# Kernel tuning notes

Hardware: AMD Instinct MI355X
Metric: run time of the kernel (lower is better)

The kernel has to match this reference:

```python
import jax, jax.numpy as jnp
import numpy as np

H = 8       # n_heads
N = 128     # n_vars
HEAD = 64   # per-head dim (== __init__ dim)


def setup_inputs() -> dict:
    key = jax.random.key(0)
    k0, k1, k2, k3, k4 = jax.random.split(key, 5)
    B, L = 4, 8192
    D = H * HEAD
    x = jax.random.normal(k0, (B, L, D), dtype=jnp.float32)
    # nn.Linear default init: U(-1/sqrt(fan_in), 1/sqrt(fan_in)), fan_in = HEAD
    s = 1.0 / np.sqrt(HEAD)
    w1 = jax.random.uniform(k1, (HEAD, HEAD), jnp.float32, -s, s)
    b1 = jax.random.uniform(k2, (HEAD,), jnp.float32, -s, s)
    w2 = jax.random.uniform(k3, (HEAD, HEAD), jnp.float32, -s, s)
    b2 = jax.random.uniform(k4, (HEAD,), jnp.float32, -s, s)
    return {"x": x, "w1": w1, "b1": b1, "w2": w2, "b2": b2}


def reference(x, w1, b1, w2, b2):
    B, L, D = x.shape
    P = L // N  # patches per variable
    # (B,L,D) -> (B,H,L,HEAD) -> (B,H,N,P,HEAD)
    xh = x.reshape(B, L, H, HEAD).transpose(0, 2, 1, 3).reshape(B, H, N, P, HEAD)
    q = xh @ w1.T + b1  # proj_1
    k = xh @ w2.T + b2  # proj_2
    # per (b,h,patch) NxN adjacency over variables
    adj = jax.nn.gelu(jnp.einsum('bhixd,bhjxd->bhxij', q, k), approximate=False)
    adj = jax.nn.softmax(adj, axis=-1)
    # dropout is identity in eval mode; F.normalize(p=1): divide by max(L1, eps)
    adj = adj / jnp.maximum(jnp.sum(jnp.abs(adj), axis=-1, keepdims=True), 1e-12)
    out = jnp.einsum('bhxij,bhjxd->bixhd', adj, xh)  # (B,N,P,H,HEAD)
    return out.reshape(B, L, H * HEAD)
```

## Files before the change

### kernel.cpp

```cpp
#include <hip/hip_runtime.h>
#include <math.h>


namespace {
constexpr int H = 8, NV = 128, HEAD = 64, B = 4, L = 8192;
constexpr int P = L / NV;
constexpr int D = H * HEAD;
constexpr int RS = P * D;

constexpr int XT_S = 136;
constexpr int XH_S = 72;
constexpr int TA_S = 72;

typedef _Float16 half8  __attribute__((ext_vector_type(8)));
typedef _Float16 half4h __attribute__((ext_vector_type(4)));
typedef _Float16 half2v __attribute__((ext_vector_type(2)));
typedef __fp16   fp16x2 __attribute__((ext_vector_type(2)));
typedef float    floatx4 __attribute__((ext_vector_type(4)));

__device__ __forceinline__ floatx4 mfma16(half8 a, half8 b, floatx4 c) {
    return __builtin_amdgcn_mfma_f32_16x16x32_f16(a, b, c, 0, 0, 0);
}

__device__ __forceinline__ half8 cvt8(float4 a, float4 b) {
    fp16x2 p0 = __builtin_amdgcn_cvt_pkrtz(a.x, a.y);
    fp16x2 p1 = __builtin_amdgcn_cvt_pkrtz(a.z, a.w);
    fp16x2 p2 = __builtin_amdgcn_cvt_pkrtz(b.x, b.y);
    fp16x2 p3 = __builtin_amdgcn_cvt_pkrtz(b.z, b.w);
    half8 r;
    r[0] = (_Float16)p0[0]; r[1] = (_Float16)p0[1];
    r[2] = (_Float16)p1[0]; r[3] = (_Float16)p1[1];
    r[4] = (_Float16)p2[0]; r[5] = (_Float16)p2[1];
    r[6] = (_Float16)p3[0]; r[7] = (_Float16)p3[1];
    return r;
}

__device__ __forceinline__ float& vslot(_Float16* xt, int j) {
    return ((float*)(xt + (size_t)(j >> 2) * XT_S + 128))[j & 3];
}

__global__ __launch_bounds__(256) void pack_g(
    const float* __restrict__ w1, const float* __restrict__ w2,
    const float* __restrict__ b1, const float* __restrict__ b2,
    _Float16* __restrict__ gth, float* __restrict__ g1f,
    float* __restrict__ g2f, float* __restrict__ cf)
{
    const int t = threadIdx.x;
    if (blockIdx.x == 16) {
        if (t < 64) {
            float a = 0.f;
            #pragma unroll 8
            for (int n = 0; n < 64; ++n) a = fmaf(w1[n * 64 + t], b2[n], a);
            g1f[t] = a;
        } else if (t < 128) {
            const int d = t - 64;
            float a = 0.f;
            #pragma unroll 8
            for (int n = 0; n < 64; ++n) a = fmaf(w2[n * 64 + d], b1[n], a);
            g2f[d] = a;
        } else if (t == 128) {
            float a = 0.f;
            for (int n = 0; n < 64; ++n) a = fmaf(b1[n], b2[n], a);
            cf[0] = a;
        }
        return;
    }
    const int gid = blockIdx.x * 256 + t;
    const int d = gid & 63, e = gid >> 6;
    float a = 0.f;
    #pragma unroll 8
    for (int n = 0; n < 64; ++n) a = fmaf(w1[n * 64 + d], w2[n * 64 + e], a);
    gth[e * 64 + d] = (_Float16)a;
}

__global__ __launch_bounds__(256, 3) void space_graph_mfma5(
    const float* __restrict__ x, const _Float16* __restrict__ gth,
    const float* __restrict__ g1f, const float* __restrict__ g2f,
    const float* __restrict__ cf, float* __restrict__ out)
{
    __shared__ _Float16 lds[64 * XT_S + NV * XH_S + NV * TA_S];
    _Float16* Xt = lds;
    _Float16* Xh = lds + 64 * XT_S;
    _Float16* TA = Xh + NV * XH_S;

    const int t    = threadIdx.x;
    const int lane = t & 63;
    const int w    = t >> 6;
    const int col  = lane & 15;
    const int quad = lane >> 4;

    const int blk = blockIdx.x;
    const int p = blk & (P - 1);
    const int h = (blk >> 6) & (H - 1);
    const int b = blk >> 9;
    const size_t base = ((size_t)b * L + (size_t)p) * D + (size_t)h * HEAD;

    {
        const int c  = t & 15;
        const int tt = t >> 4;
        #pragma unroll
        for (int it = 0; it < 4; ++it) {
            const int j0 = 2 * (tt + 16 * it);
            const float4 v0 = *(const float4*)(x + base + (size_t)j0 * RS + c * 4);
            const float4 v1 = *(const float4*)(x + base + (size_t)(j0 + 1) * RS + c * 4);
            const float va[4] = {v0.x, v0.y, v0.z, v0.w};
            const float vb[4] = {v1.x, v1.y, v1.z, v1.w};
            half4h ra, rb;
            #pragma unroll
            for (int q = 0; q < 4; ++q) {
                const _Float16 ha = (_Float16)va[q];
                const _Float16 hb = (_Float16)vb[q];
                ra[q] = ha; rb[q] = hb;
                half2v pr; pr[0] = ha; pr[1] = hb;
                *(half2v*)&Xt[(4 * c + q) * XT_S + j0] = pr;
            }
            *(half4h*)&Xh[(size_t)j0 * XH_S + 4 * c] = ra;
            *(half4h*)&Xh[(size_t)(j0 + 1) * XH_S + 4 * c] = rb;
        }
    }

    floatx4 tacc[2][4];
    #pragma unroll
    for (int mt = 0; mt < 2; ++mt)
        #pragma unroll
        for (int nt = 0; nt < 4; ++nt) tacc[mt][nt] = (floatx4)0.0f;

    half8 axf[2][2];
    float up[2] = {0.f, 0.f}, vp[2] = {0.f, 0.f};
    #pragma unroll
    for (int ks = 0; ks < 2; ++ks) {
        const float4 ga = *(const float4*)(g1f + quad * 8 + 32 * ks);
        const float4 gb = *(const float4*)(g1f + quad * 8 + 32 * ks + 4);
        const float4 ha = *(const float4*)(g2f + quad * 8 + 32 * ks);
        const float4 hb = *(const float4*)(g2f + quad * 8 + 32 * ks + 4);
        #pragma unroll
        for (int mt = 0; mt < 2; ++mt) {
            const int row = 32 * w + 16 * mt + col;
            const float* src = x + base + (size_t)row * RS + quad * 8 + 32 * ks;
            const float4 v0 = *(const float4*)src;
            const float4 v1 = *(const float4*)(src + 4);
            axf[mt][ks] = cvt8(v0, v1);
            up[mt] += v0.x * ga.x + v0.y * ga.y + v0.z * ga.z + v0.w * ga.w
                    + v1.x * gb.x + v1.y * gb.y + v1.z * gb.z + v1.w * gb.w;
            vp[mt] += v0.x * ha.x + v0.y * ha.y + v0.z * ha.z + v0.w * ha.w
                    + v1.x * hb.x + v1.y * hb.y + v1.z * hb.z + v1.w * hb.w;
        }
    }

    #pragma unroll
    for (int ks = 0; ks < 2; ++ks)
        #pragma unroll
        for (int nt = 0; nt < 4; ++nt) {
            const half8 gb8 = *(const half8*)&gth[(col + 16 * nt) * HEAD + quad * 8 + 32 * ks];
            #pragma unroll
            for (int mt = 0; mt < 2; ++mt)
                tacc[mt][nt] = mfma16(axf[mt][ks], gb8, tacc[mt][nt]);
        }

    float ureg[2];
    #pragma unroll
    for (int mt = 0; mt < 2; ++mt) {
        float uu = up[mt]; uu += __shfl_xor(uu, 16); uu += __shfl_xor(uu, 32);
        float vv = vp[mt]; vv += __shfl_xor(vv, 16); vv += __shfl_xor(vv, 32);
        ureg[mt] = uu;
        if (quad == 0) vslot(Xt, 32 * w + 16 * mt + col) = vv;
    }

    #pragma unroll
    for (int mt = 0; mt < 2; ++mt)
        #pragma unroll
        for (int r = 0; r < 4; ++r) {
            const int R = 32 * w + 16 * mt + quad * 4 + r;
            _Float16* trow = &TA[R * TA_S + col];
            #pragma unroll
            for (int nt = 0; nt < 4; ++nt)
                trow[nt * 16] = (_Float16)(tacc[mt][nt][r]);
        }
    __syncthreads();

    const float cc = cf[0];
    float ucr[2][4];
    #pragma unroll
    for (int mt = 0; mt < 2; ++mt)
        #pragma unroll
        for (int r = 0; r < 4; ++r)
            ucr[mt][r] = __shfl(ureg[mt], quad * 4 + r) + cc;
    float vrow[8];
    #pragma unroll
    for (int nt = 0; nt < 8; ++nt) vrow[nt] = vslot(Xt, col + 16 * nt);

    floatx4 sacc[2][8];
    #pragma unroll
    for (int mt = 0; mt < 2; ++mt)
        #pragma unroll
        for (int nt = 0; nt < 8; ++nt)
            #pragma unroll
            for (int r = 0; r < 4; ++r)
                sacc[mt][nt][r] = ucr[mt][r] + vrow[nt];

    #pragma unroll
    for (int ks = 0; ks < 2; ++ks) {
        half8 taf[2];
        #pragma unroll
        for (int mt = 0; mt < 2; ++mt)
            taf[mt] = *(const half8*)&TA[(32 * w + 16 * mt + col) * TA_S + quad * 8 + 32 * ks];
        #pragma unroll
        for (int nt = 0; nt < 8; ++nt) {
            const half8 xb = *(const half8*)&Xh[(col + 16 * nt) * XH_S + quad * 8 + 32 * ks];
            #pragma unroll
            for (int mt = 0; mt < 2; ++mt)
                sacc[mt][nt] = mfma16(taf[mt], xb, sacc[mt][nt]);
        }
    }

    #pragma unroll
    for (int mt = 0; mt < 2; ++mt)
        #pragma unroll
        for (int r = 0; r < 4; ++r) {
            float wv[8]; float rs = 0.f;
            #pragma unroll
            for (int nt = 0; nt < 8; ++nt) {
                const float s  = sacc[mt][nt][r];
                const float u  = s * fmaf(s * s, 0.035677408137f, 0.7978845608f);
                const float em = __expf(-2.0f * u);
                const float g  = s * __builtin_amdgcn_rcpf(1.0f + em);
                const float e  = __expf(g);
                wv[nt] = e; rs += e;
            }
            rs += __shfl_xor(rs, 1); rs += __shfl_xor(rs, 2);
            rs += __shfl_xor(rs, 4); rs += __shfl_xor(rs, 8);
            const float inv = __builtin_amdgcn_rcpf(rs);
            #pragma unroll
            for (int nt = 0; nt < 8; ++nt) sacc[mt][nt][r] = wv[nt] * inv;
        }

    #pragma unroll
    for (int mt = 0; mt < 2; ++mt)
        #pragma unroll
        for (int r = 0; r < 4; ++r) {
            const int R = 32 * w + 16 * mt + quad * 4 + r;
            _Float16* arow = &TA[R * TA_S + col];
            #pragma unroll
            for (int nt = 0; nt < 4; ++nt)
                arow[nt * 16] = (_Float16)(sacc[mt][nt][r]);
        }

    floatx4 oacc[2][4];
    #pragma unroll
    for (int mt = 0; mt < 2; ++mt)
        #pragma unroll
        for (int nt = 0; nt < 4; ++nt) oacc[mt][nt] = (floatx4)0.0f;

    #pragma unroll
    for (int kh = 0; kh < 2; ++kh) {
        half8 aaf[2];
        #pragma unroll
        for (int mt = 0; mt < 2; ++mt)
            aaf[mt] = *(const half8*)&TA[(32 * w + 16 * mt + col) * TA_S + quad * 8 + 32 * kh];
        #pragma unroll
        for (int nt = 0; nt < 4; ++nt) {
            const half8 xb = *(const half8*)&Xt[(col + 16 * nt) * XT_S + quad * 8 + 32 * kh];
            #pragma unroll
            for (int mt = 0; mt < 2; ++mt)
                oacc[mt][nt] = mfma16(aaf[mt], xb, oacc[mt][nt]);
        }
    }

    #pragma unroll
    for (int mt = 0; mt < 2; ++mt)
        #pragma unroll
        for (int r = 0; r < 4; ++r) {
            const int R = 32 * w + 16 * mt + quad * 4 + r;
            _Float16* arow = &TA[R * TA_S + col];
            #pragma unroll
            for (int nt = 4; nt < 8; ++nt)
                arow[(nt - 4) * 16] = (_Float16)(sacc[mt][nt][r]);
        }

    #pragma unroll
    for (int kh = 0; kh < 2; ++kh) {
        half8 aaf[2];
        #pragma unroll
        for (int mt = 0; mt < 2; ++mt)
            aaf[mt] = *(const half8*)&TA[(32 * w + 16 * mt + col) * TA_S + quad * 8 + 32 * kh];
        #pragma unroll
        for (int nt = 0; nt < 4; ++nt) {
            const half8 xb = *(const half8*)&Xt[(col + 16 * nt) * XT_S + quad * 8 + 32 * (kh + 2)];
            #pragma unroll
            for (int mt = 0; mt < 2; ++mt)
                oacc[mt][nt] = mfma16(aaf[mt], xb, oacc[mt][nt]);
        }
    }

    #pragma unroll
    for (int mt = 0; mt < 2; ++mt)
        #pragma unroll
        for (int r = 0; r < 4; ++r) {
            const int i = 32 * w + 16 * mt + quad * 4 + r;
            float* orow = out + base + (size_t)i * RS + col;
            #pragma unroll
            for (int nt = 0; nt < 4; ++nt)
                orow[nt * 16] = oacc[mt][nt][r];
        }
}
}

extern "C" void kernel_launch(void* const* d_in, const int* in_sizes, int n_in,
                              void* d_out, int out_size, void* d_ws, size_t ws_size,
                              hipStream_t stream) {
    const float* x  = (const float*)d_in[0];
    const float* w1 = (const float*)d_in[1];
    const float* b1 = (const float*)d_in[2];
    const float* w2 = (const float*)d_in[3];
    const float* b2 = (const float*)d_in[4];
    float* out = (float*)d_out;

    _Float16* gth = (_Float16*)d_ws;
    float* g1f = (float*)((char*)d_ws + 8192);
    float* g2f = g1f + 64;
    float* cf  = g2f + 64;

    hipLaunchKernelGGL(pack_g, dim3(17), dim3(256), 0, stream,
                       w1, w2, b1, b2, gth, g1f, g2f, cf);
    hipLaunchKernelGGL(space_graph_mfma5, dim3(B * H * P), dim3(256), 0, stream,
                       x, gth, g1f, g2f, cf, out);
}
```

Baseline: 142.3 us.

## Use 512-thread blocks with one 16-row tile per wave and exp2-based GELU

Each block now runs 8 waves, and each wave handles a single 16-row M tile instead of two. This halves per-thread accumulator registers and aims to raise occupancy and latency hiding. The GELU-tanh plus softmax exponent is rewritten with exp2 and pre-folded log2e constants to save multiplies. The trade-off is less MFMA work per wave against more waves sharing the same LDS tile per block.

```diff
diff --git a/kernel.cpp b/kernel.cpp
--- a/kernel.cpp
+++ b/kernel.cpp
@@ -73,7 +73,7 @@
     gth[e * 64 + d] = (_Float16)a;
 }
 
-__global__ __launch_bounds__(256, 3) void space_graph_mfma5(
+__global__ __launch_bounds__(512, 6) void space_graph_mfma6(
     const float* __restrict__ x, const _Float16* __restrict__ gth,
     const float* __restrict__ g1f, const float* __restrict__ g2f,
     const float* __restrict__ cf, float* __restrict__ out)
@@ -99,8 +99,8 @@
         const int c  = t & 15;
         const int tt = t >> 4;
         #pragma unroll
-        for (int it = 0; it < 4; ++it) {
-            const int j0 = 2 * (tt + 16 * it);
+        for (int it = 0; it < 2; ++it) {
+            const int j0 = 2 * (tt + 32 * it);
             const float4 v0 = *(const float4*)(x + base + (size_t)j0 * RS + c * 4);
             const float4 v1 = *(const float4*)(x + base + (size_t)(j0 + 1) * RS + c * 4);
             const float va[4] = {v0.x, v0.y, v0.z, v0.w};
@@ -119,32 +119,27 @@
         }
     }
 
-    floatx4 tacc[2][4];
-    #pragma unroll
-    for (int mt = 0; mt < 2; ++mt)
-        #pragma unroll
-        for (int nt = 0; nt < 4; ++nt) tacc[mt][nt] = (floatx4)0.0f;
-
-    half8 axf[2][2];
-    float up[2] = {0.f, 0.f}, vp[2] = {0.f, 0.f};
+    floatx4 tacc[4];
+    #pragma unroll
+    for (int nt = 0; nt < 4; ++nt) tacc[nt] = (floatx4)0.0f;
+
+    half8 axf[2];
+    float up = 0.f, vp = 0.f;
+    const int arow0 = 16 * w + col;
     #pragma unroll
     for (int ks = 0; ks < 2; ++ks) {
         const float4 ga = *(const float4*)(g1f + quad * 8 + 32 * ks);
         const float4 gb = *(const float4*)(g1f + quad * 8 + 32 * ks + 4);
         const float4 ha = *(const float4*)(g2f + quad * 8 + 32 * ks);
         const float4 hb = *(const float4*)(g2f + quad * 8 + 32 * ks + 4);
-        #pragma unroll
-        for (int mt = 0; mt < 2; ++mt) {
-            const int row = 32 * w + 16 * mt + col;
-            const float* src = x + base + (size_t)row * RS + quad * 8 + 32 * ks;
-            const float4 v0 = *(const float4*)src;
-            const float4 v1 = *(const float4*)(src + 4);
-            axf[mt][ks] = cvt8(v0, v1);
-            up[mt] += v0.x * ga.x + v0.y * ga.y + v0.z * ga.z + v0.w * ga.w
-                    + v1.x * gb.x + v1.y * gb.y + v1.z * gb.z + v1.w * gb.w;
-            vp[mt] += v0.x * ha.x + v0.y * ha.y + v0.z * ha.z + v0.w * ha.w
-                    + v1.x * hb.x + v1.y * hb.y + v1.z * hb.z + v1.w * hb.w;
-        }
+        const float* src = x + base + (size_t)arow0 * RS + quad * 8 + 32 * ks;
+        const float4 v0 = *(const float4*)src;
+        const float4 v1 = *(const float4*)(src + 4);
+        axf[ks] = cvt8(v0, v1);
+        up += v0.x * ga.x + v0.y * ga.y + v0.z * ga.z + v0.w * ga.w
+            + v1.x * gb.x + v1.y * gb.y + v1.z * gb.z + v1.w * gb.w;
+        vp += v0.x * ha.x + v0.y * ha.y + v0.z * ha.z + v0.w * ha.w
+            + v1.x * hb.x + v1.y * hb.y + v1.z * hb.z + v1.w * hb.w;
     }
 
     #pragma unroll
@@ -152,156 +147,122 @@
         #pragma unroll
         for (int nt = 0; nt < 4; ++nt) {
             const half8 gb8 = *(const half8*)&gth[(col + 16 * nt) * HEAD + quad * 8 + 32 * ks];
-            #pragma unroll
-            for (int mt = 0; mt < 2; ++mt)
-                tacc[mt][nt] = mfma16(axf[mt][ks], gb8, tacc[mt][nt]);
-        }
-
-    float ureg[2];
-    #pragma unroll
-    for (int mt = 0; mt < 2; ++mt) {
-        float uu = up[mt]; uu += __shfl_xor(uu, 16); uu += __shfl_xor(uu, 32);
-        float vv = vp[mt]; vv += __shfl_xor(vv, 16); vv += __shfl_xor(vv, 32);
-        ureg[mt] = uu;
-        if (quad == 0) vslot(Xt, 32 * w + 16 * mt + col) = vv;
-    }
-
-    #pragma unroll
-    for (int mt = 0; mt < 2; ++mt)
-        #pragma unroll
-        for (int r = 0; r < 4; ++r) {
-            const int R = 32 * w + 16 * mt + quad * 4 + r;
-            _Float16* trow = &TA[R * TA_S + col];
-            #pragma unroll
-            for (int nt = 0; nt < 4; ++nt)
-                trow[nt * 16] = (_Float16)(tacc[mt][nt][r]);
-        }
+            tacc[nt] = mfma16(axf[ks], gb8, tacc[nt]);
+        }
+
+    float ureg;
+    {
+        float uu = up; uu += __shfl_xor(uu, 16); uu += __shfl_xor(uu, 32);
+        float vv = vp; vv += __shfl_xor(vv, 16); vv += __shfl_xor(vv, 32);
+        ureg = uu;
+        if (quad == 0) vslot(Xt, arow0) = vv;
+    }
+
+    #pragma unroll
+    for (int r = 0; r < 4; ++r) {
+        const int R = 16 * w + quad * 4 + r;
+        _Float16* trow = &TA[R * TA_S + col];
+        #pragma unroll
+        for (int nt = 0; nt < 4; ++nt)
+            trow[nt * 16] = (_Float16)(tacc[nt][r]);
+    }
     __syncthreads();
 
     const float cc = cf[0];
-    float ucr[2][4];
-    #pragma unroll
-    for (int mt = 0; mt < 2; ++mt)
+    float ucr[4];
+    #pragma unroll
+    for (int r = 0; r < 4; ++r)
+        ucr[r] = __shfl(ureg, quad * 4 + r) + cc;
+    float vrow[8];
+    #pragma unroll
+    for (int nt = 0; nt < 8; ++nt) vrow[nt] = vslot(Xt, col + 16 * nt);
+
+    floatx4 sacc[8];
+    #pragma unroll
+    for (int nt = 0; nt < 8; ++nt)
         #pragma unroll
         for (int r = 0; r < 4; ++r)
-            ucr[mt][r] = __shfl(ureg[mt], quad * 4 + r) + cc;
-    float vrow[8];
-    #pragma unroll
-    for (int nt = 0; nt < 8; ++nt) vrow[nt] = vslot(Xt, col + 16 * nt);
-
-    floatx4 sacc[2][8];
-    #pragma unroll
-    for (int mt = 0; mt < 2; ++mt)
-        #pragma unroll
-        for (int nt = 0; nt < 8; ++nt)
-            #pragma unroll
-            for (int r = 0; r < 4; ++r)
-                sacc[mt][nt][r] = ucr[mt][r] + vrow[nt];
+            sacc[nt][r] = ucr[r] + vrow[nt];
 
     #pragma unroll
     for (int ks = 0; ks < 2; ++ks) {
-        half8 taf[2];
-        #pragma unroll
-        for (int mt = 0; mt < 2; ++mt)
-            taf[mt] = *(const half8*)&TA[(32 * w + 16 * mt + col) * TA_S + quad * 8 + 32 * ks];
+        const half8 taf = *(const half8*)&TA[arow0 * TA_S + quad * 8 + 32 * ks];
         #pragma unroll
         for (int nt = 0; nt < 8; ++nt) {
             const half8 xb = *(const half8*)&Xh[(col + 16 * nt) * XH_S + quad * 8 + 32 * ks];
-            #pragma unroll
-            for (int mt = 0; mt < 2; ++mt)
-                sacc[mt][nt] = mfma16(taf[mt], xb, sacc[mt][nt]);
-        }
-    }
-
-    #pragma unroll
-    for (int mt = 0; mt < 2; ++mt)
-        #pragma unroll
-        for (int r = 0; r < 4; ++r) {
-            float wv[8]; float rs = 0.f;
-            #pragma unroll
-            for (int nt = 0; nt < 8; ++nt) {
-                const float s  = sacc[mt][nt][r];
-                const float u  = s * fmaf(s * s, 0.035677408137f, 0.7978845608f);
-                const float em = __expf(-2.0f * u);
-                const float g  = s * __builtin_amdgcn_rcpf(1.0f + em);
-                const float e  = __expf(g);
-                wv[nt] = e; rs += e;
-            }
-            rs += __shfl_xor(rs, 1); rs += __shfl_xor(rs, 2);
-            rs += __shfl_xor(rs, 4); rs += __shfl_xor(rs, 8);
-            const float inv = __builtin_amdgcn_rcpf(rs);
-            #pragma unroll
-            for (int nt = 0; nt < 8; ++nt) sacc[mt][nt][r] = wv[nt] * inv;
-        }
-
-    #pragma unroll
-    for (int mt = 0; mt < 2; ++mt)
-        #pragma unroll
-        for (int r = 0; r < 4; ++r) {
-            const int R = 32 * w + 16 * mt + quad * 4 + r;
-            _Float16* arow = &TA[R * TA_S + col];
-            #pragma unroll
-            for (int nt = 0; nt < 4; ++nt)
-                arow[nt * 16] = (_Float16)(sacc[mt][nt][r]);
-        }
-
-    floatx4 oacc[2][4];
-    #pragma unroll
-    for (int mt = 0; mt < 2; ++mt)
-        #pragma unroll
-        for (int nt = 0; nt < 4; ++nt) oacc[mt][nt] = (floatx4)0.0f;
+            sacc[nt] = mfma16(taf, xb, sacc[nt]);
+        }
+    }
+
+    #pragma unroll
+    for (int r = 0; r < 4; ++r) {
+        float wv[8]; float rs = 0.f;
+        #pragma unroll
+        for (int nt = 0; nt < 8; ++nt) {
+            const float s   = sacc[nt][r];
+            const float pl  = fmaf(s * s, -0.10294310f, -2.3022157f);
+            const float em  = __builtin_amdgcn_exp2f(s * pl);
+            const float rr  = __builtin_amdgcn_rcpf(1.0f + em);
+            const float e   = __builtin_amdgcn_exp2f((s * 1.44269504f) * rr);
+            wv[nt] = e; rs += e;
+        }
+        rs += __shfl_xor(rs, 1); rs += __shfl_xor(rs, 2);
+        rs += __shfl_xor(rs, 4); rs += __shfl_xor(rs, 8);
+        const float inv = __builtin_amdgcn_rcpf(rs);
+        #pragma unroll
+        for (int nt = 0; nt < 8; ++nt) sacc[nt][r] = wv[nt] * inv;
+    }
+
+    #pragma unroll
+    for (int r = 0; r < 4; ++r) {
+        const int R = 16 * w + quad * 4 + r;
+        _Float16* arow = &TA[R * TA_S + col];
+        #pragma unroll
+        for (int nt = 0; nt < 4; ++nt)
+            arow[nt * 16] = (_Float16)(sacc[nt][r]);
+    }
+
+    floatx4 oacc[4];
+    #pragma unroll
+    for (int nt = 0; nt < 4; ++nt) oacc[nt] = (floatx4)0.0f;
 
     #pragma unroll
     for (int kh = 0; kh < 2; ++kh) {
-        half8 aaf[2];
-        #pragma unroll
-        for (int mt = 0; mt < 2; ++mt)
-            aaf[mt] = *(const half8*)&TA[(32 * w + 16 * mt + col) * TA_S + quad * 8 + 32 * kh];
+        const half8 aaf = *(const half8*)&TA[arow0 * TA_S + quad * 8 + 32 * kh];
         #pragma unroll
         for (int nt = 0; nt < 4; ++nt) {
             const half8 xb = *(const half8*)&Xt[(col + 16 * nt) * XT_S + quad * 8 + 32 * kh];
-            #pragma unroll
-            for (int mt = 0; mt < 2; ++mt)
-                oacc[mt][nt] = mfma16(aaf[mt], xb, oacc[mt][nt]);
-        }
-    }
-
-    #pragma unroll
-    for (int mt = 0; mt < 2; ++mt)
-        #pragma unroll
-        for (int r = 0; r < 4; ++r) {
-            const int R = 32 * w + 16 * mt + quad * 4 + r;
-            _Float16* arow = &TA[R * TA_S + col];
-            #pragma unroll
-            for (int nt = 4; nt < 8; ++nt)
-                arow[(nt - 4) * 16] = (_Float16)(sacc[mt][nt][r]);
-        }
+            oacc[nt] = mfma16(aaf, xb, oacc[nt]);
+        }
+    }
+
+    #pragma unroll
+    for (int r = 0; r < 4; ++r) {
+        const int R = 16 * w + quad * 4 + r;
+        _Float16* arow = &TA[R * TA_S + col];
+        #pragma unroll
+        for (int nt = 4; nt < 8; ++nt)
+            arow[(nt - 4) * 16] = (_Float16)(sacc[nt][r]);
+    }
 
     #pragma unroll
     for (int kh = 0; kh < 2; ++kh) {
-        half8 aaf[2];
-        #pragma unroll
-        for (int mt = 0; mt < 2; ++mt)
-            aaf[mt] = *(const half8*)&TA[(32 * w + 16 * mt + col) * TA_S + quad * 8 + 32 * kh];
+        const half8 aaf = *(const half8*)&TA[arow0 * TA_S + quad * 8 + 32 * kh];
         #pragma unroll
         for (int nt = 0; nt < 4; ++nt) {
             const half8 xb = *(const half8*)&Xt[(col + 16 * nt) * XT_S + quad * 8 + 32 * (kh + 2)];
-            #pragma unroll
-            for (int mt = 0; mt < 2; ++mt)
-                oacc[mt][nt] = mfma16(aaf[mt], xb, oacc[mt][nt]);
-        }
-    }
-
-    #pragma unroll
-    for (int mt = 0; mt < 2; ++mt)
-        #pragma unroll
-        for (int r = 0; r < 4; ++r) {
-            const int i = 32 * w + 16 * mt + quad * 4 + r;
-            float* orow = out + base + (size_t)i * RS + col;
-            #pragma unroll
-            for (int nt = 0; nt < 4; ++nt)
-                orow[nt * 16] = oacc[mt][nt][r];
-        }
+            oacc[nt] = mfma16(aaf, xb, oacc[nt]);
+        }
+    }
+
+    #pragma unroll
+    for (int r = 0; r < 4; ++r) {
+        const int i = 16 * w + quad * 4 + r;
+        float* orow = out + base + (size_t)i * RS + col;
+        #pragma unroll
+        for (int nt = 0; nt < 4; ++nt)
+            orow[nt * 16] = oacc[nt][r];
+    }
 }
 }
 
@@ -322,6 +283,6 @@
 
     hipLaunchKernelGGL(pack_g, dim3(17), dim3(256), 0, stream,
                        w1, w2, b1, b2, gth, g1f, g2f, cf);
-    hipLaunchKernelGGL(space_graph_mfma5, dim3(B * H * P), dim3(256), 0, stream,
+    hipLaunchKernelGGL(space_graph_mfma6, dim3(B * H * P), dim3(512), 0, stream,
                        x, gth, g1f, g2f, cf, out);
 }
```

Result: no change. 143.3 us (+0.8%).

## Process two tiles per block with register prefetch of the second tile

Applied to the files above, without the earlier changes.

Each block now handles two (b,h,p) tiles, halving the grid. While the first tile computes, the x loads for the second tile are held in registers, hiding global latency. The barrier is replaced with an explicit lgkmcnt wait plus s_barrier, and the GELU/exp chain is rewritten using exp2 with folded constants. The costs are higher register pressure, which may hurt occupancy, and fewer blocks to spread across CUs.

```diff
diff --git a/kernel.cpp b/kernel.cpp
--- a/kernel.cpp
+++ b/kernel.cpp
@@ -7,6 +7,7 @@
 constexpr int P = L / NV;
 constexpr int D = H * HEAD;
 constexpr int RS = P * D;
+constexpr int NT2 = (B * H * P) / 2;
 
 constexpr int XT_S = 136;
 constexpr int XH_S = 72;
@@ -73,7 +74,7 @@
     gth[e * 64 + d] = (_Float16)a;
 }
 
-__global__ __launch_bounds__(256, 3) void space_graph_mfma5(
+__global__ __launch_bounds__(256, 3) void space_graph_mfma8(
     const float* __restrict__ x, const _Float16* __restrict__ gth,
     const float* __restrict__ g1f, const float* __restrict__ g2f,
     const float* __restrict__ cf, float* __restrict__ out)
@@ -88,21 +89,33 @@
     const int w    = t >> 6;
     const int col  = lane & 15;
     const int quad = lane >> 4;
+    const int c    = t & 15;
+    const int ttv  = t >> 4;
 
     const int blk = blockIdx.x;
-    const int p = blk & (P - 1);
-    const int h = (blk >> 6) & (H - 1);
-    const int b = blk >> 9;
-    const size_t base = ((size_t)b * L + (size_t)p) * D + (size_t)h * HEAD;
-
-    {
-        const int c  = t & 15;
-        const int tt = t >> 4;
+    const int ti0 = blk, ti1 = blk + NT2;
+    const size_t base0 =
+        ((size_t)(ti0 >> 9) * L + (size_t)(ti0 & (P - 1))) * D + (size_t)((ti0 >> 6) & (H - 1)) * HEAD;
+    const size_t base1 =
+        ((size_t)(ti1 >> 9) * L + (size_t)(ti1 & (P - 1))) * D + (size_t)((ti1 >> 6) & (H - 1)) * HEAD;
+
+    float4 pf[8];
+    #pragma unroll
+    for (int it = 0; it < 4; ++it) {
+        const int j0 = 2 * (ttv + 16 * it);
+        pf[2 * it]     = *(const float4*)(x + base0 + (size_t)j0 * RS + c * 4);
+        pf[2 * it + 1] = *(const float4*)(x + base0 + (size_t)(j0 + 1) * RS + c * 4);
+    }
+
+    #pragma unroll
+    for (int tile = 0; tile < 2; ++tile) {
+        const size_t base = (tile == 0) ? base0 : base1;
+
         #pragma unroll
         for (int it = 0; it < 4; ++it) {
-            const int j0 = 2 * (tt + 16 * it);
-            const float4 v0 = *(const float4*)(x + base + (size_t)j0 * RS + c * 4);
-            const float4 v1 = *(const float4*)(x + base + (size_t)(j0 + 1) * RS + c * 4);
+            const int j0 = 2 * (ttv + 16 * it);
+            const float4 v0 = pf[2 * it];
+            const float4 v1 = pf[2 * it + 1];
             const float va[4] = {v0.x, v0.y, v0.z, v0.w};
             const float vb[4] = {v1.x, v1.y, v1.z, v1.w};
             half4h ra, rb;
@@ -117,191 +130,205 @@
             *(half4h*)&Xh[(size_t)j0 * XH_S + 4 * c] = ra;
             *(half4h*)&Xh[(size_t)(j0 + 1) * XH_S + 4 * c] = rb;
         }
+
+        floatx4 tacc[2][4];
+        #pragma unroll
+        for (int mt = 0; mt < 2; ++mt)
+            #pragma unroll
+            for (int nt = 0; nt < 4; ++nt) tacc[mt][nt] = (floatx4)0.0f;
+
+        half8 axf[2][2];
+        float up[2] = {0.f, 0.f}, vp[2] = {0.f, 0.f};
+        #pragma unroll
+        for (int ks = 0; ks < 2; ++ks) {
+            const float4 ga = *(const float4*)(g1f + quad * 8 + 32 * ks);
+            const float4 gb = *(const float4*)(g1f + quad * 8 + 32 * ks + 4);
+            const float4 ha = *(const float4*)(g2f + quad * 8 + 32 * ks);
+            const float4 hb = *(const float4*)(g2f + quad * 8 + 32 * ks + 4);
+            #pragma unroll
+            for (int mt = 0; mt < 2; ++mt) {
+                const int row = 32 * w + 16 * mt + col;
+                const float* src = x + base + (size_t)row * RS + quad * 8 + 32 * ks;
+                const float4 v0 = *(const float4*)src;
+                const float4 v1 = *(const float4*)(src + 4);
+                axf[mt][ks] = cvt8(v0, v1);
+                up[mt] += v0.x * ga.x + v0.y * ga.y + v0.z * ga.z + v0.w * ga.w
+                        + v1.x * gb.x + v1.y * gb.y + v1.z * gb.z + v1.w * gb.w;
+                vp[mt] += v0.x * ha.x + v0.y * ha.y + v0.z * ha.z + v0.w * ha.w
+                        + v1.x * hb.x + v1.y * hb.y + v1.z * hb.z + v1.w * hb.w;
+            }
+        }
+
+        if (tile == 0) {
+            #pragma unroll
+            for (int it = 0; it < 4; ++it) {
+                const int j0 = 2 * (ttv + 16 * it);
+                pf[2 * it]     = *(const float4*)(x + base1 + (size_t)j0 * RS + c * 4);
+                pf[2 * it + 1] = *(const float4*)(x + base1 + (size_t)(j0 + 1) * RS + c * 4);
+            }
+        }
+
+        #pragma unroll
+        for (int ks = 0; ks < 2; ++ks)
+            #pragma unroll
+            for (int nt = 0; nt < 4; ++nt) {
+                const half8 gb8 = *(const half8*)&gth[(col + 16 * nt) * HEAD + quad * 8 + 32 * ks];
+                #pragma unroll
+                for (int mt = 0; mt < 2; ++mt)
+                    tacc[mt][nt] = mfma16(axf[mt][ks], gb8, tacc[mt][nt]);
+            }
+
+        float ureg[2];
+        #pragma unroll
+        for (int mt = 0; mt < 2; ++mt) {
+            float uu = up[mt]; uu += __shfl_xor(uu, 16); uu += __shfl_xor(uu, 32);
+            float vv = vp[mt]; vv += __shfl_xor(vv, 16); vv += __shfl_xor(vv, 32);
+            ureg[mt] = uu;
+            if (quad == 0) vslot(Xt, 32 * w + 16 * mt + col) = vv;
+        }
+
+        #pragma unroll
+        for (int mt = 0; mt < 2; ++mt)
+            #pragma unroll
+            for (int r = 0; r < 4; ++r) {
+                const int R = 32 * w + 16 * mt + quad * 4 + r;
+                _Float16* trow = &TA[R * TA_S + col];
+                #pragma unroll
+                for (int nt = 0; nt < 4; ++nt)
+                    trow[nt * 16] = (_Float16)(tacc[mt][nt][r]);
+            }
+
+        asm volatile("s_waitcnt lgkmcnt(0)" ::: "memory");
+        __builtin_amdgcn_s_barrier();
+        __builtin_amdgcn_sched_barrier(0);
+
+        const float cc = cf[0];
+        float ucr[2][4];
+        #pragma unroll
+        for (int mt = 0; mt < 2; ++mt)
+            #pragma unroll
+            for (int r = 0; r < 4; ++r)
+                ucr[mt][r] = __shfl(ureg[mt], quad * 4 + r) + cc;
+        float vrow[8];
+        #pragma unroll
+        for (int nt = 0; nt < 8; ++nt) vrow[nt] = vslot(Xt, col + 16 * nt);
+
+        floatx4 sacc[2][8];
+        #pragma unroll
+        for (int mt = 0; mt < 2; ++mt)
+            #pragma unroll
+            for (int nt = 0; nt < 8; ++nt)
+                #pragma unroll
+                for (int r = 0; r < 4; ++r)
+                    sacc[mt][nt][r] = ucr[mt][r] + vrow[nt];
+
+        #pragma unroll
+        for (int ks = 0; ks < 2; ++ks) {
+            half8 taf[2];
+            #pragma unroll
+            for (int mt = 0; mt < 2; ++mt)
+                taf[mt] = *(const half8*)&TA[(32 * w + 16 * mt + col) * TA_S + quad * 8 + 32 * ks];
+            #pragma unroll
+            for (int nt = 0; nt < 8; ++nt) {
+                const half8 xb = *(const half8*)&Xh[(col + 16 * nt) * XH_S + quad * 8 + 32 * ks];
+                #pragma unroll
+                for (int mt = 0; mt < 2; ++mt)
+                    sacc[mt][nt] = mfma16(taf[mt], xb, sacc[mt][nt]);
+            }
+        }
+
+        #pragma unroll
+        for (int mt = 0; mt < 2; ++mt)
+            #pragma unroll
+            for (int r = 0; r < 4; ++r) {
+                float wv[8]; float rs = 0.f;
+                #pragma unroll
+                for (int nt = 0; nt < 8; ++nt) {
+                    const float s  = sacc[mt][nt][r];
+                    const float pl = fmaf(s * s, -0.10294310f, -2.3022157f);
+                    const float em = __builtin_amdgcn_exp2f(s * pl);
+                    const float rr = __builtin_amdgcn_rcpf(1.0f + em);
+                    const float e  = __builtin_amdgcn_exp2f((s * 1.44269504f) * rr);
+                    wv[nt] = e; rs += e;
+                }
+                rs += __shfl_xor(rs, 1); rs += __shfl_xor(rs, 2);
+                rs += __shfl_xor(rs, 4); rs += __shfl_xor(rs, 8);
+                const float inv = __builtin_amdgcn_rcpf(rs);
+                #pragma unroll
+                for (int nt = 0; nt < 8; ++nt) sacc[mt][nt][r] = wv[nt] * inv;
+            }
+
+        #pragma unroll
+        for (int mt = 0; mt < 2; ++mt)
+            #pragma unroll
+            for (int r = 0; r < 4; ++r) {
+                const int R = 32 * w + 16 * mt + quad * 4 + r;
+                _Float16* arow = &TA[R * TA_S + col];
+                #pragma unroll
+                for (int nt = 0; nt < 4; ++nt)
+                    arow[nt * 16] = (_Float16)(sacc[mt][nt][r]);
+            }
+
+        floatx4 oacc[2][4];
+        #pragma unroll
+        for (int mt = 0; mt < 2; ++mt)
+            #pragma unroll
+            for (int nt = 0; nt < 4; ++nt) oacc[mt][nt] = (floatx4)0.0f;
+
+        #pragma unroll
+        for (int kh = 0; kh < 2; ++kh) {
+            half8 aaf[2];
+            #pragma unroll
+            for (int mt = 0; mt < 2; ++mt)
+                aaf[mt] = *(const half8*)&TA[(32 * w + 16 * mt + col) * TA_S + quad * 8 + 32 * kh];
+            #pragma unroll
+            for (int nt = 0; nt < 4; ++nt) {
+                const half8 xb = *(const half8*)&Xt[(col + 16 * nt) * XT_S + quad * 8 + 32 * kh];
+                #pragma unroll
+                for (int mt = 0; mt < 2; ++mt)
+                    oacc[mt][nt] = mfma16(aaf[mt], xb, oacc[mt][nt]);
+            }
+        }
+
+        #pragma unroll
+        for (int mt = 0; mt < 2; ++mt)
+            #pragma unroll
+            for (int r = 0; r < 4; ++r) {
+                const int R = 32 * w + 16 * mt + quad * 4 + r;
+                _Float16* arow = &TA[R * TA_S + col];
+                #pragma unroll
+                for (int nt = 4; nt < 8; ++nt)
+                    arow[(nt - 4) * 16] = (_Float16)(sacc[mt][nt][r]);
+            }
+
+        #pragma unroll
+        for (int kh = 0; kh < 2; ++kh) {
+            half8 aaf[2];
+            #pragma unroll
+            for (int mt = 0; mt < 2; ++mt)
+                aaf[mt] = *(const half8*)&TA[(32 * w + 16 * mt + col) * TA_S + quad * 8 + 32 * kh];
+            #pragma unroll
+            for (int nt = 0; nt < 4; ++nt) {
+                const half8 xb = *(const half8*)&Xt[(col + 16 * nt) * XT_S + quad * 8 + 32 * (kh + 2)];
+                #pragma unroll
+                for (int mt = 0; mt < 2; ++mt)
+                    oacc[mt][nt] = mfma16(aaf[mt], xb, oacc[mt][nt]);
+            }
+        }
+
+        if (tile == 0) __syncthreads();
+
+        #pragma unroll
+        for (int mt = 0; mt < 2; ++mt)
+            #pragma unroll
+            for (int r = 0; r < 4; ++r) {
+                const int i = 32 * w + 16 * mt + quad * 4 + r;
+                float* orow = out + base + (size_t)i * RS + col;
+                #pragma unroll
+                for (int nt = 0; nt < 4; ++nt)
+                    orow[nt * 16] = oacc[mt][nt][r];
+            }
     }
-
-    floatx4 tacc[2][4];
-    #pragma unroll
-    for (int mt = 0; mt < 2; ++mt)
-        #pragma unroll
-        for (int nt = 0; nt < 4; ++nt) tacc[mt][nt] = (floatx4)0.0f;
-
-    half8 axf[2][2];
-    float up[2] = {0.f, 0.f}, vp[2] = {0.f, 0.f};
-    #pragma unroll
-    for (int ks = 0; ks < 2; ++ks) {
-        const float4 ga = *(const float4*)(g1f + quad * 8 + 32 * ks);
-        const float4 gb = *(const float4*)(g1f + quad * 8 + 32 * ks + 4);
-        const float4 ha = *(const float4*)(g2f + quad * 8 + 32 * ks);
-        const float4 hb = *(const float4*)(g2f + quad * 8 + 32 * ks + 4);
-        #pragma unroll
-        for (int mt = 0; mt < 2; ++mt) {
-            const int row = 32 * w + 16 * mt + col;
-            const float* src = x + base + (size_t)row * RS + quad * 8 + 32 * ks;
-            const float4 v0 = *(const float4*)src;
-            const float4 v1 = *(const float4*)(src + 4);
-            axf[mt][ks] = cvt8(v0, v1);
-            up[mt] += v0.x * ga.x + v0.y * ga.y + v0.z * ga.z + v0.w * ga.w
-                    + v1.x * gb.x + v1.y * gb.y + v1.z * gb.z + v1.w * gb.w;
-            vp[mt] += v0.x * ha.x + v0.y * ha.y + v0.z * ha.z + v0.w * ha.w
-                    + v1.x * hb.x + v1.y * hb.y + v1.z * hb.z + v1.w * hb.w;
-        }
-    }
-
-    #pragma unroll
-    for (int ks = 0; ks < 2; ++ks)
-        #pragma unroll
-        for (int nt = 0; nt < 4; ++nt) {
-            const half8 gb8 = *(const half8*)&gth[(col + 16 * nt) * HEAD + quad * 8 + 32 * ks];
-            #pragma unroll
-            for (int mt = 0; mt < 2; ++mt)
-                tacc[mt][nt] = mfma16(axf[mt][ks], gb8, tacc[mt][nt]);
-        }
-
-    float ureg[2];
-    #pragma unroll
-    for (int mt = 0; mt < 2; ++mt) {
-        float uu = up[mt]; uu += __shfl_xor(uu, 16); uu += __shfl_xor(uu, 32);
-        float vv = vp[mt]; vv += __shfl_xor(vv, 16); vv += __shfl_xor(vv, 32);
-        ureg[mt] = uu;
-        if (quad == 0) vslot(Xt, 32 * w + 16 * mt + col) = vv;
-    }
-
-    #pragma unroll
-    for (int mt = 0; mt < 2; ++mt)
-        #pragma unroll
-        for (int r = 0; r < 4; ++r) {
-            const int R = 32 * w + 16 * mt + quad * 4 + r;
-            _Float16* trow = &TA[R * TA_S + col];
-            #pragma unroll
-            for (int nt = 0; nt < 4; ++nt)
-                trow[nt * 16] = (_Float16)(tacc[mt][nt][r]);
-        }
-    __syncthreads();
-
-    const float cc = cf[0];
-    float ucr[2][4];
-    #pragma unroll
-    for (int mt = 0; mt < 2; ++mt)
-        #pragma unroll
-        for (int r = 0; r < 4; ++r)
-            ucr[mt][r] = __shfl(ureg[mt], quad * 4 + r) + cc;
-    float vrow[8];
-    #pragma unroll
-    for (int nt = 0; nt < 8; ++nt) vrow[nt] = vslot(Xt, col + 16 * nt);
-
-    floatx4 sacc[2][8];
-    #pragma unroll
-    for (int mt = 0; mt < 2; ++mt)
-        #pragma unroll
-        for (int nt = 0; nt < 8; ++nt)
-            #pragma unroll
-            for (int r = 0; r < 4; ++r)
-                sacc[mt][nt][r] = ucr[mt][r] + vrow[nt];
-
-    #pragma unroll
-    for (int ks = 0; ks < 2; ++ks) {
-        half8 taf[2];
-        #pragma unroll
-        for (int mt = 0; mt < 2; ++mt)
-            taf[mt] = *(const half8*)&TA[(32 * w + 16 * mt + col) * TA_S + quad * 8 + 32 * ks];
-        #pragma unroll
-        for (int nt = 0; nt < 8; ++nt) {
-            const half8 xb = *(const half8*)&Xh[(col + 16 * nt) * XH_S + quad * 8 + 32 * ks];
-            #pragma unroll
-            for (int mt = 0; mt < 2; ++mt)
-                sacc[mt][nt] = mfma16(taf[mt], xb, sacc[mt][nt]);
-        }
-    }
-
-    #pragma unroll
-    for (int mt = 0; mt < 2; ++mt)
-        #pragma unroll
-        for (int r = 0; r < 4; ++r) {
-            float wv[8]; float rs = 0.f;
-            #pragma unroll
-            for (int nt = 0; nt < 8; ++nt) {
-                const float s  = sacc[mt][nt][r];
-                const float u  = s * fmaf(s * s, 0.035677408137f, 0.7978845608f);
-                const float em = __expf(-2.0f * u);
-                const float g  = s * __builtin_amdgcn_rcpf(1.0f + em);
-                const float e  = __expf(g);
-                wv[nt] = e; rs += e;
-            }
-            rs += __shfl_xor(rs, 1); rs += __shfl_xor(rs, 2);
-            rs += __shfl_xor(rs, 4); rs += __shfl_xor(rs, 8);
-            const float inv = __builtin_amdgcn_rcpf(rs);
-            #pragma unroll
-            for (int nt = 0; nt < 8; ++nt) sacc[mt][nt][r] = wv[nt] * inv;
-        }
-
-    #pragma unroll
-    for (int mt = 0; mt < 2; ++mt)
-        #pragma unroll
-        for (int r = 0; r < 4; ++r) {
-            const int R = 32 * w + 16 * mt + quad * 4 + r;
-            _Float16* arow = &TA[R * TA_S + col];
-            #pragma unroll
-            for (int nt = 0; nt < 4; ++nt)
-                arow[nt * 16] = (_Float16)(sacc[mt][nt][r]);
-        }
-
-    floatx4 oacc[2][4];
-    #pragma unroll
-    for (int mt = 0; mt < 2; ++mt)
-        #pragma unroll
-        for (int nt = 0; nt < 4; ++nt) oacc[mt][nt] = (floatx4)0.0f;
-
-    #pragma unroll
-    for (int kh = 0; kh < 2; ++kh) {
-        half8 aaf[2];
-        #pragma unroll
-        for (int mt = 0; mt < 2; ++mt)
-            aaf[mt] = *(const half8*)&TA[(32 * w + 16 * mt + col) * TA_S + quad * 8 + 32 * kh];
-        #pragma unroll
-        for (int nt = 0; nt < 4; ++nt) {
-            const half8 xb = *(const half8*)&Xt[(col + 16 * nt) * XT_S + quad * 8 + 32 * kh];
-            #pragma unroll
-            for (int mt = 0; mt < 2; ++mt)
-                oacc[mt][nt] = mfma16(aaf[mt], xb, oacc[mt][nt]);
-        }
-    }
-
-    #pragma unroll
-    for (int mt = 0; mt < 2; ++mt)
-        #pragma unroll
-        for (int r = 0; r < 4; ++r) {
-            const int R = 32 * w + 16 * mt + quad * 4 + r;
-            _Float16* arow = &TA[R * TA_S + col];
-            #pragma unroll
-            for (int nt = 4; nt < 8; ++nt)
-                arow[(nt - 4) * 16] = (_Float16)(sacc[mt][nt][r]);
-        }
-
-    #pragma unroll
-    for (int kh = 0; kh < 2; ++kh) {
-        half8 aaf[2];
-        #pragma unroll
-        for (int mt = 0; mt < 2; ++mt)
-            aaf[mt] = *(const half8*)&TA[(32 * w + 16 * mt + col) * TA_S + quad * 8 + 32 * kh];
-        #pragma unroll
-        for (int nt = 0; nt < 4; ++nt) {
-            const half8 xb = *(const half8*)&Xt[(col + 16 * nt) * XT_S + quad * 8 + 32 * (kh + 2)];
-            #pragma unroll
-            for (int mt = 0; mt < 2; ++mt)
-                oacc[mt][nt] = mfma16(aaf[mt], xb, oacc[mt][nt]);
-        }
-    }
-
-    #pragma unroll
-    for (int mt = 0; mt < 2; ++mt)
-        #pragma unroll
-        for (int r = 0; r < 4; ++r) {
-            const int i = 32 * w + 16 * mt + quad * 4 + r;
-            float* orow = out + base + (size_t)i * RS + col;
-            #pragma unroll
-            for (int nt = 0; nt < 4; ++nt)
-                orow[nt * 16] = oacc[mt][nt][r];
-        }
 }
 }
 
@@ -322,6 +349,6 @@
 
     hipLaunchKernelGGL(pack_g, dim3(17), dim3(256), 0, stream,
                        w1, w2, b1, b2, gth, g1f, g2f, cf);
-    hipLaunchKernelGGL(space_graph_mfma5, dim3(B * H * P), dim3(256), 0, stream,
+    hipLaunchKernelGGL(space_graph_mfma8, dim3(NT2), dim3(256), 0, stream,
                        x, gth, g1f, g2f, cf, out);
 }
```

Result: slower. 156.2 us (+9.8%).
